# Performance work log

Hardware: AMD Instinct MI355X
Metric: run time of the kernel (lower is better)

Reference implementation:

```python
import jax, jax.numpy as jnp
import numpy as np

B, T, C, DU, OUT = 16, 2048, 1024, 1024, 512
CIF_THRESHOLD = 1.0


def setup_inputs():
    key = jax.random.key(0)
    k0, k1, k2, k3, k4, k5 = jax.random.split(key, 6)
    encoder_out = jax.random.normal(k0, (B, T, C), dtype=jnp.float32)
    input_lengths = (T // 2 + jax.random.randint(k1, (B,), 0, T // 2)).astype(jnp.int32)
    target_lengths = (200 + jax.random.randint(k2, (B,), 0, 300)).astype(jnp.int32)
    s = 1.0 / np.sqrt(C)
    Wd = jax.random.uniform(k3, (DU, C), jnp.float32, -s, s)
    bd = jnp.zeros((DU,), jnp.float32)
    sp = 1.0 / np.sqrt(DU)
    Wp = jax.random.uniform(k4, (1, DU), jnp.float32, -sp, sp)
    bp = jnp.zeros((1,), jnp.float32)
    Wo = jax.random.uniform(k5, (OUT, C), jnp.float32, -s, s)
    return {"encoder_out": encoder_out, "input_lengths": input_lengths,
            "target_lengths": target_lengths, "Wd": Wd, "bd": bd,
            "Wp": Wp, "bp": bp, "Wo": Wo}


def _cif_forward(encoder_out, input_lengths, target_lengths, Wd, bd, Wp, bp, Wo):
    Bsz, Tlen, Cdim = encoder_out.shape
    pos = jnp.arange(Tlen)
    not_pad = (pos[None, :] < input_lengths[:, None]).astype(encoder_out.dtype)  # [B,T]

    # dense weight production: relu(x Wd^T + bd) -> sigmoid(. Wp^T + bp)
    h = jax.nn.relu(jnp.einsum('btc,dc->btd', encoder_out, Wd) + bd)
    weight = jax.nn.sigmoid(jnp.einsum('btd,od->bto', h, Wp)[..., 0] + bp[0])
    org_weight = weight * not_pad

    # training-time scaling so weights sum to target_lengths
    scale = target_lengths.astype(encoder_out.dtype) / (org_weight.sum(-1) + 1e-8)
    weight = org_weight * scale[:, None]

    padding_start_id = input_lengths  # = not_padding_mask.sum(-1)

    def step(carry, xs):
        acc_w, acc_s = carry                     # [B], [B,C]
        w, e, i = xs                             # [B], [B,C], scalar step idx
        fired = (acc_w + w) >= CIF_THRESHOLD     # [B]
        remained = 1.0 - acc_w
        new_w = jnp.where(fired, w - remained, w + acc_w)
        new_s = jnp.where(fired[:, None], (w - remained)[:, None] * e,
                          acc_s + w[:, None] * e)
        f_s = jnp.where(fired[:, None], acc_s + remained[:, None] * e, 0.0)
        f_s = jnp.where((i > padding_start_id)[:, None], 0.0, f_s)
        return (new_w, new_s), f_s

    init = (jnp.zeros((Bsz,), encoder_out.dtype),
            jnp.zeros((Bsz, Cdim), encoder_out.dtype))
    _, fired_states = jax.lax.scan(
        step, init,
        (weight.T, jnp.transpose(encoder_out, (1, 0, 2)), jnp.arange(Tlen)))
    fired_states = jnp.transpose(fired_states, (1, 0, 2))  # [B,T,C]

    fired_marks = jnp.abs(fired_states).sum(-1) != 0.0     # [B,T]
    # stable-compact fired frames to front; pad to T (upper bound of fired_max_length)
    order = jnp.argsort(jnp.logical_not(fired_marks).astype(jnp.int32), axis=1)
    n_fired = fired_marks.sum(-1)                           # [B]
    valid = pos[None, :] < n_fired[:, None]                 # [B,T]
    cif_outputs = jnp.take_along_axis(fired_states, order[:, :, None], axis=1)
    cif_outputs = cif_outputs * valid[:, :, None].astype(cif_outputs.dtype)

    idx = jnp.where(valid, order, 0).astype(jnp.int32)
    prev = jnp.concatenate([jnp.zeros((Bsz, 1), jnp.int32), idx[:, :-1]], axis=1)
    cif_durations = (idx - prev) * valid.astype(jnp.int32)

    base_mask = (pos[None, :] == 0).astype(jnp.int32)       # [1,0,0,...] fallback
    cif_out_padding_mask = jnp.where((n_fired > 0)[:, None],
                                     valid.astype(jnp.int32), base_mask)
    quantity_out = org_weight.sum(-1)                       # training branch
    cif_outputs = jnp.einsum('btc,oc->bto', cif_outputs, Wo)  # bias-free output proj
    return cif_outputs, cif_out_padding_mask, cif_durations, quantity_out


def reference(encoder_out, input_lengths, target_lengths, Wd, bd, Wp, bp, Wo):
    return _cif_forward(encoder_out, input_lengths, target_lengths,
                        Wd, bd, Wp, bp, Wo)
```

## Files before the change

kernel.cpp:

```cpp
#include <hip/hip_runtime.h>
#include <cstdint>
#include <cstddef>

#define BSZ 16
#define TLEN 2048
#define CDIM 1024
#define OUTDIM 512
#define MAXF 512

typedef _Float16 f16x8 __attribute__((ext_vector_type(8)));
typedef _Float16 f16x4 __attribute__((ext_vector_type(4)));
typedef float f32x16 __attribute__((ext_vector_type(16)));

__device__ __forceinline__ void gl_lds16(const void* g, void* l) {
    __builtin_amdgcn_global_load_lds(
        (const __attribute__((address_space(1))) void*)g,
        (__attribute__((address_space(3))) void*)l, 16, 0, 0);
}

struct h2pair { _Float16 h0, h1; };
__device__ __forceinline__ h2pair split2(float a) {
    h2pair o;
    o.h0 = (_Float16)a;
    float r = a - (float)o.h0;
    o.h1 = (_Float16)(r * 2048.0f);
    return o;
}

__global__ __launch_bounds__(128) void k0a_split_wd(
    const float* __restrict__ Wd, _Float16* __restrict__ B0,
    _Float16* __restrict__ B1)
{
    const int dut = blockIdx.x;
    const int ktl = blockIdx.y;
    const int r = threadIdx.x;
    const float* src = Wd + (size_t)(dut * 128 + r) * CDIM + ktl * 32;
    float v[32];
#pragma unroll
    for (int j = 0; j < 8; j++) *(float4*)&v[j * 4] = *(const float4*)(src + j * 4);
    const size_t tb = (size_t)(dut * 32 + ktl) * 4096;
#pragma unroll
    for (int c = 0; c < 4; c++) {
        f16x8 h0, h1;
#pragma unroll
        for (int j = 0; j < 8; j++) {
            h2pair s = split2(v[c * 8 + j]);
            h0[j] = s.h0;
            h1[j] = s.h1;
        }
        *(f16x8*)&B0[tb + (c * 128 + r) * 8] = h0;
        *(f16x8*)&B1[tb + (c * 128 + r) * 8] = h1;
    }
}

__global__ __launch_bounds__(256) void k0c_split_wo(
    const float* __restrict__ Wo, _Float16* __restrict__ W0,
    _Float16* __restrict__ W1)
{
    const int i = (blockIdx.x * 256 + threadIdx.x) * 4;
    float4 v = *(const float4*)(Wo + i);
    f16x4 h0, h1;
    h2pair s0 = split2(v.x); h0[0] = s0.h0; h1[0] = s0.h1;
    h2pair s1 = split2(v.y); h0[1] = s1.h0; h1[1] = s1.h1;
    h2pair s2 = split2(v.z); h0[2] = s2.h0; h1[2] = s2.h1;
    h2pair s3 = split2(v.w); h0[3] = s3.h0; h1[3] = s3.h1;
    *(f16x4*)&W0[i] = h0;
    *(f16x4*)&W1[i] = h1;
}

__global__ __launch_bounds__(256, 2) void k1_weight_gemm(
    const float* __restrict__ enc, const _Float16* __restrict__ BT0,
    const _Float16* __restrict__ BT1, const float* __restrict__ bd,
    const float* __restrict__ Wp, float* __restrict__ g)
{
    __shared__ __align__(16) _Float16 lds[32768];

    const int tid = threadIdx.x;
    const int lane = tid & 63;
    const int wv = tid >> 6;
    const int l5 = lane & 31;
    const int hi = lane >> 5;
    const int mtb = (wv & 1) * 64;
    const int ntb = (wv >> 1) * 64;

    const int bx = blockIdx.x;
    const int xcd = bx & 7;
    const int j = bx >> 3;
    const int rg = xcd * 32 + (j >> 3);
    const int du = j & 7;
    const long row0 = (long)rg * 128;
    const int du0 = du * 128;

    const int sr = tid >> 1;
    const int sh = tid & 1;
    const float* aptr = enc + (row0 + sr) * (long)CDIM + sh * 16;

    const _Float16* btile = ((wv >> 1) ? BT1 : BT0) + (size_t)du * 32 * 4096;
    const int bh = wv & 1;
    const int bofs = 8192 + (wv >> 1) * 4096 + bh * 2048;

    f32x16 acc[2][2], accc[2][2];
#pragma unroll
    for (int mt = 0; mt < 2; mt++)
#pragma unroll
        for (int nt = 0; nt < 2; nt++)
#pragma unroll
            for (int r = 0; r < 16; r++) { acc[mt][nt][r] = 0.f; accc[mt][nt][r] = 0.f; }

    float fa[16];

#pragma unroll
    for (int jj = 0; jj < 4; jj++)
        *(float4*)&fa[jj * 4] = *(const float4*)(aptr + jj * 4);
    {
        f16x8 va0[2], va1[2];
#pragma unroll
        for (int c = 0; c < 2; c++)
#pragma unroll
            for (int jj = 0; jj < 8; jj++) {
                h2pair s = split2(fa[c * 8 + jj]);
                va0[c][jj] = s.h0;
                va1[c][jj] = s.h1;
            }
#pragma unroll
        for (int c = 0; c < 2; c++) {
            *(f16x8*)&lds[((sh * 2 + c) * 128 + sr) * 8] = va0[c];
            *(f16x8*)&lds[4096 + ((sh * 2 + c) * 128 + sr) * 8] = va1[c];
        }
#pragma unroll
        for (int c = 0; c < 4; c++)
            gl_lds16(btile + (bh * 256 + c * 64 + lane) * 8,
                     &lds[bofs + c * 512]);
    }
#pragma unroll
    for (int jj = 0; jj < 4; jj++)
        *(float4*)&fa[jj * 4] = *(const float4*)(aptr + 32 + jj * 4);

    for (int kt = 0; kt < 32; ++kt) {
        const int cur = (kt & 1) * 16384;
        const int nxt = ((kt & 1) ^ 1) * 16384;

        __syncthreads();

        if (kt < 31) {
#pragma unroll
            for (int c = 0; c < 4; c++)
                gl_lds16(btile + (size_t)(kt + 1) * 4096 + (bh * 256 + c * 64 + lane) * 8,
                         &lds[nxt + bofs + c * 512]);
            f16x8 va0[2], va1[2];
#pragma unroll
            for (int c = 0; c < 2; c++)
#pragma unroll
                for (int jj = 0; jj < 8; jj++) {
                    h2pair s = split2(fa[c * 8 + jj]);
                    va0[c][jj] = s.h0;
                    va1[c][jj] = s.h1;
                }
#pragma unroll
            for (int c = 0; c < 2; c++) {
                *(f16x8*)&lds[nxt + ((sh * 2 + c) * 128 + sr) * 8] = va0[c];
                *(f16x8*)&lds[nxt + 4096 + ((sh * 2 + c) * 128 + sr) * 8] = va1[c];
            }
            if (kt < 30) {
#pragma unroll
                for (int jj = 0; jj < 4; jj++)
                    *(float4*)&fa[jj * 4] = *(const float4*)(aptr + (kt + 2) * 32 + jj * 4);
            }
        }

#pragma unroll
        for (int ks = 0; ks < 2; ks++) {
            const int ch = ks * 2 + hi;
            f16x8 A0[2], A1[2], B0[2], B1[2];
#pragma unroll
            for (int mt = 0; mt < 2; mt++) {
                const int row = mtb + mt * 32 + l5;
                A0[mt] = *(const f16x8*)&lds[cur + (ch * 128 + row) * 8];
                A1[mt] = *(const f16x8*)&lds[cur + 4096 + (ch * 128 + row) * 8];
            }
#pragma unroll
            for (int nt = 0; nt < 2; nt++) {
                const int row = ntb + nt * 32 + l5;
                B0[nt] = *(const f16x8*)&lds[cur + 8192 + (ch * 128 + row) * 8];
                B1[nt] = *(const f16x8*)&lds[cur + 12288 + (ch * 128 + row) * 8];
            }
#pragma unroll
            for (int mt = 0; mt < 2; mt++)
#pragma unroll
                for (int nt = 0; nt < 2; nt++) {
                    acc[mt][nt] = __builtin_amdgcn_mfma_f32_32x32x16_f16(
                        A0[mt], B0[nt], acc[mt][nt], 0, 0, 0);
                    accc[mt][nt] = __builtin_amdgcn_mfma_f32_32x32x16_f16(
                        A0[mt], B1[nt], accc[mt][nt], 0, 0, 0);
                    accc[mt][nt] = __builtin_amdgcn_mfma_f32_32x32x16_f16(
                        A1[mt], B0[nt], accc[mt][nt], 0, 0, 0);
                }
        }
    }

    float bdv[2], wpv[2];
#pragma unroll
    for (int nt = 0; nt < 2; nt++) {
        int n = du0 + ntb + nt * 32 + l5;
        bdv[nt] = bd[n];
        wpv[nt] = Wp[n];
    }
    float pm[2][16];
#pragma unroll
    for (int mt = 0; mt < 2; mt++)
#pragma unroll
        for (int r = 0; r < 16; r++) {
            float s = 0.f;
#pragma unroll
            for (int nt = 0; nt < 2; nt++) {
                float h = acc[mt][nt][r] + 4.8828125e-4f * accc[mt][nt][r] + bdv[nt];
                h = h > 0.f ? h : 0.f;
                s += wpv[nt] * h;
            }
            s += __shfl_xor(s, 1);
            s += __shfl_xor(s, 2);
            s += __shfl_xor(s, 4);
            s += __shfl_xor(s, 8);
            s += __shfl_xor(s, 16);
            pm[mt][r] = s;
        }
    float out = 0.f;
#pragma unroll
    for (int mt = 0; mt < 2; mt++)
#pragma unroll
        for (int r = 0; r < 16; r++)
            if (l5 == mt * 16 + r) out = pm[mt][r];
    const int mt_sel = l5 >> 4;
    const int r_sel = l5 & 15;
    const int row = mtb + mt_sel * 32 + (r_sel & 3) + 8 * (r_sel >> 2) + 4 * hi;
    atomicAdd(&g[row0 + row], out);
}

__global__ __launch_bounds__(256) void k2_scan(
    const float* __restrict__ g, const int* __restrict__ in_len,
    const int* __restrict__ tgt_len, const float* __restrict__ bp,
    float* __restrict__ c_a, float* __restrict__ c_b,
    int* __restrict__ fire_t, int* __restrict__ n_fired,
    float* __restrict__ out_mask, float* __restrict__ out_dur,
    float* __restrict__ out_qty)
{
    __shared__ float w[TLEN];
    __shared__ float ca[TLEN];
    __shared__ float cb[TLEN];
    __shared__ int fires[MAXF];
    __shared__ float ssum[256];
    __shared__ float s_scale;
    __shared__ int s_nf;

    const int b = blockIdx.x;
    const int tid = threadIdx.x;
    const int len = in_len[b];
    const float bpv = bp[0];

    float local = 0.f;
    for (int t = tid; t < TLEN; t += 256) {
        float gv = g[b * TLEN + t] + bpv;
        float s = 1.f / (1.f + expf(-gv));
        float ow = (t < len) ? s : 0.f;
        w[t] = ow;
        local += ow;
    }
    ssum[tid] = local;
    __syncthreads();
    for (int st = 128; st > 0; st >>= 1) {
        if (tid < st) ssum[tid] += ssum[tid + st];
        __syncthreads();
    }
    if (tid == 0) {
        float org_sum = ssum[0];
        out_qty[b] = org_sum;
        s_scale = (float)tgt_len[b] / (org_sum + 1e-8f);
    }
    __syncthreads();
    float scale = s_scale;
    for (int t = tid; t < TLEN; t += 256) w[t] *= scale;
    __syncthreads();

    if (tid == 0) {
        float accw = 0.f;
        int k = 0;
        int t = 0;
        for (; t + 8 <= len; t += 8) {
            float4 wa = *(const float4*)&w[t];
            float4 wb4 = *(const float4*)&w[t + 4];
            float wv8[8] = {wa.x, wa.y, wa.z, wa.w, wb4.x, wb4.y, wb4.z, wb4.w};
#pragma unroll
            for (int u = 0; u < 8; u++) {
                float wt = wv8[u];
                float aw = accw + wt;
                bool f = (aw >= 1.0f);
                float rem = 1.0f - accw;
                float fb = wt - rem;
                ca[t + u] = f ? rem : wt;
                cb[t + u] = f ? fb : 0.f;
                fires[k & (MAXF - 1)] = t + u;
                k += f ? 1 : 0;
                accw = f ? fb : aw;
            }
        }
        for (; t < len; t++) {
            float wt = w[t];
            float aw = accw + wt;
            bool f = (aw >= 1.0f);
            float rem = 1.0f - accw;
            float fb = wt - rem;
            ca[t] = f ? rem : wt;
            cb[t] = f ? fb : 0.f;
            fires[k & (MAXF - 1)] = t;
            k += f ? 1 : 0;
            accw = f ? fb : aw;
        }
        s_nf = (k < MAXF) ? k : MAXF;
        n_fired[b] = s_nf;
    }
    __syncthreads();

    for (int t = tid; t < len; t += 256) {
        c_a[b * TLEN + t] = ca[t];
        c_b[b * TLEN + t] = cb[t];
    }
    const int nf = s_nf;
    for (int jj = tid; jj < nf; jj += 256) {
        int tj = fires[jj];
        fire_t[b * MAXF + jj] = tj;
        out_mask[b * TLEN + jj] = 1.0f;
        int prev = (jj == 0) ? 0 : fires[jj - 1];
        out_dur[b * TLEN + jj] = (float)(tj - prev);
    }
    if (tid == 0 && nf == 0) out_mask[b * TLEN] = 1.0f;
}

__global__ __launch_bounds__(256) void k3a_compact(
    const float* __restrict__ enc, const float* __restrict__ c_a,
    const float* __restrict__ c_b, const int* __restrict__ fire_t,
    const int* __restrict__ n_fired, _Float16* __restrict__ C0,
    _Float16* __restrict__ C1)
{
    const int b = blockIdx.y;
    const int k = blockIdx.x;
    const int tid = threadIdx.x;
    _Float16* d0 = C0 + ((size_t)b * MAXF + k) * CDIM + tid * 4;
    _Float16* d1 = C1 + ((size_t)b * MAXF + k) * CDIM + tid * 4;
    if (k >= n_fired[b]) {
        f16x4 z = {(_Float16)0.f, (_Float16)0.f, (_Float16)0.f, (_Float16)0.f};
        *(f16x4*)d0 = z;
        *(f16x4*)d1 = z;
        return;
    }
    const int tend = fire_t[b * MAXF + k];
    const int tprev = (k == 0) ? -1 : fire_t[b * MAXF + k - 1];
    float ax = 0.f, ay = 0.f, az = 0.f, aw = 0.f;
    const int tstart = (tprev < 0) ? 0 : tprev;
    for (int t = tstart; t <= tend; t++) {
        float coef = (t == tprev) ? c_b[b * TLEN + t] : c_a[b * TLEN + t];
        const float4 e = *(const float4*)(enc + ((size_t)b * TLEN + t) * CDIM + tid * 4);
        ax += coef * e.x;
        ay += coef * e.y;
        az += coef * e.z;
        aw += coef * e.w;
    }
    f16x4 h0, h1;
    h2pair s0 = split2(ax); h0[0] = s0.h0; h1[0] = s0.h1;
    h2pair s1 = split2(ay); h0[1] = s1.h0; h1[1] = s1.h1;
    h2pair s2 = split2(az); h0[2] = s2.h0; h1[2] = s2.h1;
    h2pair s3 = split2(aw); h0[3] = s3.h0; h1[3] = s3.h1;
    *(f16x4*)d0 = h0;
    *(f16x4*)d1 = h1;
}

__global__ __launch_bounds__(256, 2) void k3b_outproj(
    const _Float16* __restrict__ C0, const _Float16* __restrict__ C1,
    const _Float16* __restrict__ W0, const _Float16* __restrict__ W1,
    const int* __restrict__ n_fired, float* __restrict__ out0)
{
    __shared__ __align__(16) _Float16 lds[16384];

    const int b = blockIdx.z;
    const int nf = n_fired[b];
    const int j0 = blockIdx.x * 128;
    if (j0 >= nf) return;
    const int o0 = blockIdx.y * 128;
    const int tid = threadIdx.x;
    const int lane = tid & 63;
    const int wv = tid >> 6;
    const int l5 = lane & 31;
    const int hi = lane >> 5;
    const int mtb = (wv & 1) * 64;
    const int ntb = (wv >> 1) * 64;

    const int sr = tid >> 1;
    const int sh = tid & 1;
    const _Float16* a0p = C0 + ((size_t)b * MAXF + j0 + sr) * CDIM + sh * 16;
    const _Float16* a1p = C1 + ((size_t)b * MAXF + j0 + sr) * CDIM + sh * 16;
    const _Float16* b0p = W0 + (size_t)(o0 + sr) * CDIM + sh * 16;
    const _Float16* b1p = W1 + (size_t)(o0 + sr) * CDIM + sh * 16;

    f32x16 acc[2][2], accc[2][2];
#pragma unroll
    for (int mt = 0; mt < 2; mt++)
#pragma unroll
        for (int nt = 0; nt < 2; nt++)
#pragma unroll
            for (int r = 0; r < 16; r++) { acc[mt][nt][r] = 0.f; accc[mt][nt][r] = 0.f; }

    f16x8 xa0[2], xa1[2], xb0[2], xb1[2];
#pragma unroll
    for (int c = 0; c < 2; c++) {
        xa0[c] = *(const f16x8*)(a0p + c * 8);
        xa1[c] = *(const f16x8*)(a1p + c * 8);
        xb0[c] = *(const f16x8*)(b0p + c * 8);
        xb1[c] = *(const f16x8*)(b1p + c * 8);
    }

    for (int kt = 0; kt < 32; ++kt) {
        __syncthreads();
#pragma unroll
        for (int c = 0; c < 2; c++) {
            *(f16x8*)&lds[((sh * 2 + c) * 128 + sr) * 8] = xa0[c];
            *(f16x8*)&lds[4096 + ((sh * 2 + c) * 128 + sr) * 8] = xa1[c];
            *(f16x8*)&lds[8192 + ((sh * 2 + c) * 128 + sr) * 8] = xb0[c];
            *(f16x8*)&lds[12288 + ((sh * 2 + c) * 128 + sr) * 8] = xb1[c];
        }
        __syncthreads();
        if (kt < 31) {
            const int o = (kt + 1) * 32;
#pragma unroll
            for (int c = 0; c < 2; c++) {
                xa0[c] = *(const f16x8*)(a0p + o + c * 8);
                xa1[c] = *(const f16x8*)(a1p + o + c * 8);
                xb0[c] = *(const f16x8*)(b0p + o + c * 8);
                xb1[c] = *(const f16x8*)(b1p + o + c * 8);
            }
        }
#pragma unroll
        for (int ks = 0; ks < 2; ks++) {
            const int ch = ks * 2 + hi;
            f16x8 A0[2], A1[2], B0[2], B1[2];
#pragma unroll
            for (int mt = 0; mt < 2; mt++) {
                const int row = mtb + mt * 32 + l5;
                A0[mt] = *(const f16x8*)&lds[(ch * 128 + row) * 8];
                A1[mt] = *(const f16x8*)&lds[4096 + (ch * 128 + row) * 8];
            }
#pragma unroll
            for (int nt = 0; nt < 2; nt++) {
                const int row = ntb + nt * 32 + l5;
                B0[nt] = *(const f16x8*)&lds[8192 + (ch * 128 + row) * 8];
                B1[nt] = *(const f16x8*)&lds[12288 + (ch * 128 + row) * 8];
            }
#pragma unroll
            for (int mt = 0; mt < 2; mt++)
#pragma unroll
                for (int nt = 0; nt < 2; nt++) {
                    acc[mt][nt] = __builtin_amdgcn_mfma_f32_32x32x16_f16(
                        A0[mt], B0[nt], acc[mt][nt], 0, 0, 0);
                    accc[mt][nt] = __builtin_amdgcn_mfma_f32_32x32x16_f16(
                        A0[mt], B1[nt], accc[mt][nt], 0, 0, 0);
                    accc[mt][nt] = __builtin_amdgcn_mfma_f32_32x32x16_f16(
                        A1[mt], B0[nt], accc[mt][nt], 0, 0, 0);
                }
        }
    }

#pragma unroll
    for (int mt = 0; mt < 2; mt++)
#pragma unroll
        for (int nt = 0; nt < 2; nt++)
#pragma unroll
            for (int r = 0; r < 16; r++) {
                float val = acc[mt][nt][r] + 4.8828125e-4f * accc[mt][nt][r];
                int m = mtb + mt * 32 + (r & 3) + 8 * (r >> 2) + 4 * hi;
                int col = o0 + ntb + nt * 32 + l5;
                out0[((size_t)b * TLEN + j0 + m) * OUTDIM + col] = val;
            }
}

extern "C" void kernel_launch(void* const* d_in, const int* in_sizes, int n_in,
                              void* d_out, int out_size, void* d_ws, size_t ws_size,
                              hipStream_t stream)
{
    const float* enc = (const float*)d_in[0];
    const int* in_len = (const int*)d_in[1];
    const int* tgt_len = (const int*)d_in[2];
    const float* Wd = (const float*)d_in[3];
    const float* bd = (const float*)d_in[4];
    const float* Wp = (const float*)d_in[5];
    const float* bp = (const float*)d_in[6];
    const float* Wo = (const float*)d_in[7];

    char* ws = (char*)d_ws;
    float* g       = (float*)(ws + 0);
    float* c_a     = (float*)(ws + 131072);
    float* c_b     = (float*)(ws + 262144);
    int* fire_t    = (int*)(ws + 393216);
    int* n_fired   = (int*)(ws + 425984);
    _Float16* WdT0 = (_Float16*)(ws + 458752);
    _Float16* WdT1 = (_Float16*)(ws + 2555904);
    _Float16* Wo0  = (_Float16*)(ws + 4653056);
    _Float16* Wo1  = (_Float16*)(ws + 5701632);
    _Float16* C0   = (_Float16*)(ws + 6750208);
    _Float16* C1   = (_Float16*)(ws + 23527424);

    float* out0 = (float*)d_out;
    float* out_mask = out0 + (size_t)BSZ * TLEN * OUTDIM;
    float* out_dur = out_mask + (size_t)BSZ * TLEN;
    float* out_qty = out_dur + (size_t)BSZ * TLEN;

    (void)hipMemsetAsync(g, 0, 131072, stream);
    (void)hipMemsetAsync(d_out, 0, (size_t)out_size * 4, stream);

    k0a_split_wd<<<dim3(8, 32), 128, 0, stream>>>(Wd, WdT0, WdT1);
    k0c_split_wo<<<512, 256, 0, stream>>>(Wo, Wo0, Wo1);
    k1_weight_gemm<<<2048, 256, 0, stream>>>(enc, WdT0, WdT1, bd, Wp, g);
    k2_scan<<<BSZ, 256, 0, stream>>>(g, in_len, tgt_len, bp, c_a, c_b,
                                     fire_t, n_fired, out_mask, out_dur, out_qty);
    k3a_compact<<<dim3(MAXF, BSZ), 256, 0, stream>>>(enc, c_a, c_b, fire_t,
                                                     n_fired, C0, C1);
    k3b_outproj<<<dim3(4, 4, BSZ), 256, 0, stream>>>(C0, C1, Wo0, Wo1,
                                                     n_fired, out0);
}
```

Before: 590.8 us.

## Load Wd fragments directly to registers, fuse split kernels, zero output in projection

Wd's fp16 hi/lo split is now written in MFMA fragment order, so the weight GEMM loads B operands straight from global memory into registers instead of staging them through LDS. This halves LDS usage per block. The two weight-split kernels are merged into one launch. The full-output memset is replaced by having the output-projection kernel write zeros for unfired row tiles, using a grid that covers all time rows. Direct global B loads are now issued after the barrier and may stall the MFMAs if latency is not hidden.

```diff
diff --git a/kernel.cpp b/kernel.cpp
--- a/kernel.cpp
+++ b/kernel.cpp
@@ -11,12 +11,6 @@
 typedef _Float16 f16x8 __attribute__((ext_vector_type(8)));
 typedef _Float16 f16x4 __attribute__((ext_vector_type(4)));
 typedef float f32x16 __attribute__((ext_vector_type(16)));
-
-__device__ __forceinline__ void gl_lds16(const void* g, void* l) {
-    __builtin_amdgcn_global_load_lds(
-        (const __attribute__((address_space(1))) void*)g,
-        (__attribute__((address_space(3))) void*)l, 16, 0, 0);
-}
 
 struct h2pair { _Float16 h0, h1; };
 __device__ __forceinline__ h2pair split2(float a) {
@@ -27,20 +21,43 @@
     return o;
 }
 
-__global__ __launch_bounds__(128) void k0a_split_wd(
-    const float* __restrict__ Wd, _Float16* __restrict__ B0,
-    _Float16* __restrict__ B1)
+__global__ __launch_bounds__(128) void k0_split(
+    const float* __restrict__ Wd, const float* __restrict__ Wo,
+    _Float16* __restrict__ BF, _Float16* __restrict__ W0,
+    _Float16* __restrict__ W1)
 {
-    const int dut = blockIdx.x;
-    const int ktl = blockIdx.y;
+    const int bx = blockIdx.x;
+    const int by = blockIdx.y;
     const int r = threadIdx.x;
-    const float* src = Wd + (size_t)(dut * 128 + r) * CDIM + ktl * 32;
+
+    if (by == 32) {
+        const int lane = bx * 128 + r;
+        for (int i = 0; i < 128; i++) {
+            const int i4 = i * 1024 + lane;
+            float4 v = *(const float4*)(Wo + i4 * 4);
+            f16x4 h0, h1;
+            h2pair s0 = split2(v.x); h0[0] = s0.h0; h1[0] = s0.h1;
+            h2pair s1 = split2(v.y); h0[1] = s1.h0; h1[1] = s1.h1;
+            h2pair s2 = split2(v.z); h0[2] = s2.h0; h1[2] = s2.h1;
+            h2pair s3 = split2(v.w); h0[3] = s3.h0; h1[3] = s3.h1;
+            *(f16x4*)&W0[i4 * 4] = h0;
+            *(f16x4*)&W1[i4 * 4] = h1;
+        }
+        return;
+    }
+
+    const int dut = bx, kt = by;
+    const float* src = Wd + (size_t)(dut * 128 + r) * CDIM + kt * 32;
     float v[32];
 #pragma unroll
     for (int j = 0; j < 8; j++) *(float4*)&v[j * 4] = *(const float4*)(src + j * 4);
-    const size_t tb = (size_t)(dut * 32 + ktl) * 4096;
+
+    const int ntb2 = r >> 6, nt = (r >> 5) & 1, l5 = r & 31;
+    const size_t base = (size_t)dut * 131072 + (size_t)kt * 4096 +
+                        (size_t)ntb2 * 2048 + (size_t)nt * 512;
 #pragma unroll
     for (int c = 0; c < 4; c++) {
+        const int ks = c >> 1, hi = c & 1;
         f16x8 h0, h1;
 #pragma unroll
         for (int j = 0; j < 8; j++) {
@@ -48,32 +65,18 @@
             h0[j] = s.h0;
             h1[j] = s.h1;
         }
-        *(f16x8*)&B0[tb + (c * 128 + r) * 8] = h0;
-        *(f16x8*)&B1[tb + (c * 128 + r) * 8] = h1;
-    }
-}
-
-__global__ __launch_bounds__(256) void k0c_split_wo(
-    const float* __restrict__ Wo, _Float16* __restrict__ W0,
-    _Float16* __restrict__ W1)
+        const size_t idx = base + (size_t)ks * 1024 + (size_t)(hi * 32 + l5) * 8;
+        *(f16x8*)&BF[idx] = h0;
+        *(f16x8*)&BF[1048576 + idx] = h1;
+    }
+}
+
+__global__ __launch_bounds__(256, 2) void k1_weight_gemm(
+    const float* __restrict__ enc, const _Float16* __restrict__ BF,
+    const float* __restrict__ bd, const float* __restrict__ Wp,
+    float* __restrict__ g)
 {
-    const int i = (blockIdx.x * 256 + threadIdx.x) * 4;
-    float4 v = *(const float4*)(Wo + i);
-    f16x4 h0, h1;
-    h2pair s0 = split2(v.x); h0[0] = s0.h0; h1[0] = s0.h1;
-    h2pair s1 = split2(v.y); h0[1] = s1.h0; h1[1] = s1.h1;
-    h2pair s2 = split2(v.z); h0[2] = s2.h0; h1[2] = s2.h1;
-    h2pair s3 = split2(v.w); h0[3] = s3.h0; h1[3] = s3.h1;
-    *(f16x4*)&W0[i] = h0;
-    *(f16x4*)&W1[i] = h1;
-}
-
-__global__ __launch_bounds__(256, 2) void k1_weight_gemm(
-    const float* __restrict__ enc, const _Float16* __restrict__ BT0,
-    const _Float16* __restrict__ BT1, const float* __restrict__ bd,
-    const float* __restrict__ Wp, float* __restrict__ g)
-{
-    __shared__ __align__(16) _Float16 lds[32768];
+    __shared__ __align__(16) _Float16 lds[16384];
 
     const int tid = threadIdx.x;
     const int lane = tid & 63;
@@ -95,9 +98,8 @@
     const int sh = tid & 1;
     const float* aptr = enc + (row0 + sr) * (long)CDIM + sh * 16;
 
-    const _Float16* btile = ((wv >> 1) ? BT1 : BT0) + (size_t)du * 32 * 4096;
-    const int bh = wv & 1;
-    const int bofs = 8192 + (wv >> 1) * 4096 + bh * 2048;
+    const _Float16* bbase = BF + (size_t)du * 131072 +
+                            (size_t)(wv >> 1) * 2048 + (size_t)lane * 8;
 
     f32x16 acc[2][2], accc[2][2];
 #pragma unroll
@@ -127,26 +129,28 @@
             *(f16x8*)&lds[((sh * 2 + c) * 128 + sr) * 8] = va0[c];
             *(f16x8*)&lds[4096 + ((sh * 2 + c) * 128 + sr) * 8] = va1[c];
         }
-#pragma unroll
-        for (int c = 0; c < 4; c++)
-            gl_lds16(btile + (bh * 256 + c * 64 + lane) * 8,
-                     &lds[bofs + c * 512]);
     }
 #pragma unroll
     for (int jj = 0; jj < 4; jj++)
         *(float4*)&fa[jj * 4] = *(const float4*)(aptr + 32 + jj * 4);
 
     for (int kt = 0; kt < 32; ++kt) {
-        const int cur = (kt & 1) * 16384;
-        const int nxt = ((kt & 1) ^ 1) * 16384;
+        const int cur = (kt & 1) * 8192;
+        const int nxt = ((kt & 1) ^ 1) * 8192;
 
         __syncthreads();
 
+        f16x8 Bc[2][2][2];
+#pragma unroll
+        for (int p = 0; p < 2; p++)
+#pragma unroll
+            for (int ks = 0; ks < 2; ks++)
+#pragma unroll
+                for (int nt = 0; nt < 2; nt++)
+                    Bc[p][ks][nt] = *(const f16x8*)(bbase + (size_t)p * 1048576 +
+                                                    (size_t)kt * 4096 + ks * 1024 + nt * 512);
+
         if (kt < 31) {
-#pragma unroll
-            for (int c = 0; c < 4; c++)
-                gl_lds16(btile + (size_t)(kt + 1) * 4096 + (bh * 256 + c * 64 + lane) * 8,
-                         &lds[nxt + bofs + c * 512]);
             f16x8 va0[2], va1[2];
 #pragma unroll
             for (int c = 0; c < 2; c++)
@@ -171,7 +175,7 @@
 #pragma unroll
         for (int ks = 0; ks < 2; ks++) {
             const int ch = ks * 2 + hi;
-            f16x8 A0[2], A1[2], B0[2], B1[2];
+            f16x8 A0[2], A1[2];
 #pragma unroll
             for (int mt = 0; mt < 2; mt++) {
                 const int row = mtb + mt * 32 + l5;
@@ -179,21 +183,15 @@
                 A1[mt] = *(const f16x8*)&lds[cur + 4096 + (ch * 128 + row) * 8];
             }
 #pragma unroll
-            for (int nt = 0; nt < 2; nt++) {
-                const int row = ntb + nt * 32 + l5;
-                B0[nt] = *(const f16x8*)&lds[cur + 8192 + (ch * 128 + row) * 8];
-                B1[nt] = *(const f16x8*)&lds[cur + 12288 + (ch * 128 + row) * 8];
-            }
-#pragma unroll
             for (int mt = 0; mt < 2; mt++)
 #pragma unroll
                 for (int nt = 0; nt < 2; nt++) {
                     acc[mt][nt] = __builtin_amdgcn_mfma_f32_32x32x16_f16(
-                        A0[mt], B0[nt], acc[mt][nt], 0, 0, 0);
+                        A0[mt], Bc[0][ks][nt], acc[mt][nt], 0, 0, 0);
                     accc[mt][nt] = __builtin_amdgcn_mfma_f32_32x32x16_f16(
-                        A0[mt], B1[nt], accc[mt][nt], 0, 0, 0);
+                        A0[mt], Bc[1][ks][nt], accc[mt][nt], 0, 0, 0);
                     accc[mt][nt] = __builtin_amdgcn_mfma_f32_32x32x16_f16(
-                        A1[mt], B0[nt], accc[mt][nt], 0, 0, 0);
+                        A1[mt], Bc[0][ks][nt], accc[mt][nt], 0, 0, 0);
                 }
         }
     }
@@ -383,9 +381,20 @@
     const int b = blockIdx.z;
     const int nf = n_fired[b];
     const int j0 = blockIdx.x * 128;
-    if (j0 >= nf) return;
     const int o0 = blockIdx.y * 128;
     const int tid = threadIdx.x;
+
+    if (j0 >= nf) {
+        const float4 z = make_float4(0.f, 0.f, 0.f, 0.f);
+#pragma unroll
+        for (int i = 0; i < 16; i++) {
+            const int f = i * 256 + tid;
+            const int row = f >> 5, col4 = f & 31;
+            *(float4*)(out0 + ((size_t)b * TLEN + j0 + row) * OUTDIM + o0 + col4 * 4) = z;
+        }
+        return;
+    }
+
     const int lane = tid & 63;
     const int wv = tid >> 6;
     const int l5 = lane & 31;
@@ -499,8 +508,7 @@
     float* c_b     = (float*)(ws + 262144);
     int* fire_t    = (int*)(ws + 393216);
     int* n_fired   = (int*)(ws + 425984);
-    _Float16* WdT0 = (_Float16*)(ws + 458752);
-    _Float16* WdT1 = (_Float16*)(ws + 2555904);
+    _Float16* BF   = (_Float16*)(ws + 458752);
     _Float16* Wo0  = (_Float16*)(ws + 4653056);
     _Float16* Wo1  = (_Float16*)(ws + 5701632);
     _Float16* C0   = (_Float16*)(ws + 6750208);
@@ -512,15 +520,14 @@
     float* out_qty = out_dur + (size_t)BSZ * TLEN;
 
     (void)hipMemsetAsync(g, 0, 131072, stream);
-    (void)hipMemsetAsync(d_out, 0, (size_t)out_size * 4, stream);
-
-    k0a_split_wd<<<dim3(8, 32), 128, 0, stream>>>(Wd, WdT0, WdT1);
-    k0c_split_wo<<<512, 256, 0, stream>>>(Wo, Wo0, Wo1);
-    k1_weight_gemm<<<2048, 256, 0, stream>>>(enc, WdT0, WdT1, bd, Wp, g);
+    (void)hipMemsetAsync(out_mask, 0, (size_t)(BSZ * TLEN * 2 + BSZ) * 4, stream);
+
+    k0_split<<<dim3(8, 33), 128, 0, stream>>>(Wd, Wo, BF, Wo0, Wo1);
+    k1_weight_gemm<<<2048, 256, 0, stream>>>(enc, BF, bd, Wp, g);
     k2_scan<<<BSZ, 256, 0, stream>>>(g, in_len, tgt_len, bp, c_a, c_b,
                                      fire_t, n_fired, out_mask, out_dur, out_qty);
     k3a_compact<<<dim3(MAXF, BSZ), 256, 0, stream>>>(enc, c_a, c_b, fire_t,
                                                      n_fired, C0, C1);
-    k3b_outproj<<<dim3(4, 4, BSZ), 256, 0, stream>>>(C0, C1, Wo0, Wo1,
-                                                     n_fired, out0);
-}
+    k3b_outproj<<<dim3(16, 4, BSZ), 256, 0, stream>>>(C0, C1, Wo0, Wo1,
+                                                      n_fired, out0);
+}
```

Result: slower. 684.8 us (+15.9%).
